# Optimization experiments

Measured on AMD Instinct MI355X. Metric: run time of the kernel, lower is better.

The kernel has to match this reference:

```python
import jax, jax.numpy as jnp
import numpy as np

N_NODES = 100000
N_EDGES = 1600000
IN_CH, HID_CH, OUT_CH = 128, 128, 64


def _glorot(key, shape):
    lim = np.sqrt(6.0 / (shape[0] + shape[1])).astype(np.float32)
    return jax.random.uniform(key, shape, jnp.float32, -lim, lim)


def setup_inputs() -> dict:
    key = jax.random.key(0)
    ks = jax.random.split(key, 11)
    x = jax.random.normal(ks[0], (N_NODES, IN_CH), jnp.float32)
    edge_index = jax.random.randint(ks[1], (2, N_EDGES), 0, N_NODES, dtype=jnp.int64)
    dims = [(IN_CH, HID_CH), (HID_CH, HID_CH), (HID_CH, OUT_CH)]
    params = {}
    for i, (din, dout) in enumerate(dims):
        params[f"Wl{i}"] = _glorot(ks[2 + 3 * i], (din, dout))
        params[f"Wr{i}"] = _glorot(ks[3 + 3 * i], (din, dout))
        params[f"b{i}"] = jnp.zeros((dout,), jnp.float32)
    return {"x": x, "edge_index": edge_index, **params}


def _sage_conv(x, src, dst, Wl, Wr, b):
    # mean aggregation of neighbor (source) features at each destination node
    msg_sum = jax.ops.segment_sum(x[src], dst, num_segments=N_NODES)  # [N, din]
    deg = jax.ops.segment_sum(jnp.ones((src.shape[0],), x.dtype), dst,
                              num_segments=N_NODES)
    mean = msg_sum / jnp.maximum(deg, 1.0)[:, None]
    # lin_l(aggr) + lin_r(self), bias only in lin_l (PyG SAGEConv default)
    return mean @ Wl + x @ Wr + b


def reference(x, edge_index, Wl0, Wr0, b0, Wl1, Wr1, b1, Wl2, Wr2, b2):
    src, dst = edge_index[0], edge_index[1]
    h = jax.nn.relu(_sage_conv(x, src, dst, Wl0, Wr0, b0))  # dropout = identity (eval)
    h = jax.nn.relu(_sage_conv(h, src, dst, Wl1, Wr1, b1))
    out = _sage_conv(h, src, dst, Wl2, Wr2, b2)
    return out
```

## Files before the change

### kernel.cpp

```cpp
#include <hip/hip_runtime.h>
#include <stdint.h>

#define NN 100000
#define NE 1600000
#define NBUK 782
#define G 256
#define CHUNK 6250
#define GCHUNK 512

typedef unsigned int u32;
typedef unsigned short u16;
typedef short v8s __attribute__((ext_vector_type(8)));
typedef float v4f __attribute__((ext_vector_type(4)));

union U4S8 {
    uint4 u;
    v8s s;
};

__device__ __forceinline__ float bf2f(u16 u) {
    return __uint_as_float(((u32)u) << 16);
}
__device__ __forceinline__ u16 f2bf(float f) {
    u32 u = __float_as_uint(f);
    u = u + 0x7FFFu + ((u >> 16) & 1u);
    return (u16)(u >> 16);
}
__device__ __forceinline__ float lo16(u32 u) { return __uint_as_float(u << 16); }
__device__ __forceinline__ float hi16(u32 u) {
    return __uint_as_float(u & 0xFFFF0000u);
}

#define SL ((NN + 1) * 8)

__global__ void detect_kernel(const u32* __restrict__ ei,
                              const u32* __restrict__ x, int* flags) {
    __shared__ int bad64, badbf;
    int t = threadIdx.x;
    if (t == 0) { bad64 = 0; badbf = 0; }
    __syncthreads();
    if (ei[2 * t + 1] != 0u) atomicAdd(&bad64, 1);
    u32 d = x[t];
    u32 e = (d >> 7) & 0xFFu;
    if (e != 0u && (e < 96u || e > 160u)) atomicAdd(&badbf, 1);
    __syncthreads();
    if (t == 0) {
        flags[0] = (bad64 < 16) ? 1 : 0;
        flags[1] = (badbf < 16) ? 1 : 0;
    }
}

__global__ void conv_x(const void* __restrict__ x, const int* __restrict__ flags,
                       u32* __restrict__ xbG, u32* __restrict__ h1G,
                       u32* __restrict__ h2G) {
    int i = blockIdx.x * 256 + threadIdx.x;
    if (i >= (NN + 1) * 64) return;
    int c = i & 7;
    int q = i >> 3;
    int node = q % (NN + 1);
    int g = q / (NN + 1);
    if (node == NN) {
        xbG[i] = 0;
        h1G[i] = 0;
        h2G[i] = 0;
        return;
    }
    int col = g * 8 + c;
    u32 o;
    if (flags[1]) {
        o = ((const u32*)x)[node * 64 + col];
    } else {
        float2 v = ((const float2*)x)[node * 64 + col];
        o = ((u32)f2bf(v.y) << 16) | (u32)f2bf(v.x);
    }
    xbG[i] = o;
}

__global__ void wt_prep_all(const void* __restrict__ Wr0,
                            const void* __restrict__ Wl0,
                            const void* __restrict__ b0,
                            const void* __restrict__ Wr1,
                            const void* __restrict__ Wl1,
                            const void* __restrict__ b1,
                            const void* __restrict__ Wr2,
                            const void* __restrict__ Wl2,
                            const void* __restrict__ b2,
                            const int* __restrict__ flags,
                            u16* __restrict__ WT0, float* __restrict__ bf0,
                            u16* __restrict__ WT1, float* __restrict__ bf1,
                            u16* __restrict__ WT2, float* __restrict__ bf2_) {
    const void* Wr;
    const void* Wl;
    const void* bias;
    u16* WT;
    float* bias_f;
    int cout, t;
    if (blockIdx.x < 128) {
        Wr = Wr0; Wl = Wl0; bias = b0; WT = WT0; bias_f = bf0; cout = 128;
        t = blockIdx.x * 256 + threadIdx.x;
    } else if (blockIdx.x < 256) {
        Wr = Wr1; Wl = Wl1; bias = b1; WT = WT1; bias_f = bf1; cout = 128;
        t = (blockIdx.x - 128) * 256 + threadIdx.x;
    } else {
        Wr = Wr2; Wl = Wl2; bias = b2; WT = WT2; bias_f = bf2_; cout = 64;
        t = (blockIdx.x - 256) * 256 + threadIdx.x;
    }
    if (t < 256 * cout) {
        int k = t / cout, c = t % cout;
        const void* W = (k < 128) ? Wr : Wl;
        int kk = k & 127;
        float v;
        if (flags[1])
            v = bf2f(((const u16*)W)[kk * cout + c]);
        else
            v = ((const float*)W)[kk * cout + c];
        WT[c * 256 + k] = f2bf(v);
    }
    if (t < cout) {
        bias_f[t] =
            flags[1] ? bf2f(((const u16*)bias)[t]) : ((const float*)bias)[t];
    }
}

__global__ __launch_bounds__(256) void p1_hist(const void* __restrict__ ei,
                                               const int* __restrict__ flags,
                                               int* __restrict__ hist) {
    __shared__ int h[NBUK];
    int g = blockIdx.x, t = threadIdx.x;
    for (int b = t; b < NBUK; b += 256) h[b] = 0;
    __syncthreads();
    int e0 = g * CHUNK;
    int e1 = e0 + CHUNK;
    const int* p = (const int*)ei;
    if (flags[0]) {
        for (int e = e0 + t; e < e1; e += 256)
            atomicAdd(&h[p[2 * (NE + e)] >> 7], 1);
    } else {
        for (int e = e0 + t; e < e1; e += 256)
            atomicAdd(&h[p[NE + e] >> 7], 1);
    }
    __syncthreads();
    for (int b = t; b < NBUK; b += 256) hist[b * G + g] = h[b];
}

__global__ void scan_block_g(const int* __restrict__ in, int* __restrict__ out,
                             int* __restrict__ bsums, int n) {
    __shared__ int sS[256];
    int t = threadIdx.x;
    int base = blockIdx.x * 1024 + t * 4;
    int c[4];
#pragma unroll
    for (int i = 0; i < 4; ++i) c[i] = (base + i < n) ? in[base + i] : 0;
    int s = c[0] + c[1] + c[2] + c[3];
    sS[t] = s;
    __syncthreads();
    for (int dlt = 1; dlt < 256; dlt <<= 1) {
        int v = (t >= dlt) ? sS[t - dlt] : 0;
        __syncthreads();
        sS[t] += v;
        __syncthreads();
    }
    int run = sS[t] - s;
    if (t == 255) bsums[blockIdx.x] = sS[255];
#pragma unroll
    for (int i = 0; i < 4; ++i) {
        if (base + i < n) out[base + i] = run;
        run += c[i];
    }
}

__global__ void scan_top_g(int* bsums, int nb) {
    __shared__ int sS[256];
    int t = threadIdx.x;
    int v = (t < nb) ? bsums[t] : 0;
    sS[t] = v;
    __syncthreads();
    for (int d = 1; d < 256; d <<= 1) {
        int u = (t >= d) ? sS[t - d] : 0;
        __syncthreads();
        sS[t] += u;
        __syncthreads();
    }
    if (t < nb) bsums[t] = sS[t] - v;
}

__global__ void scan_add_g(int* __restrict__ out, const int* __restrict__ bsums,
                           int n) {
    int i = blockIdx.x * 256 + threadIdx.x;
    if (i < n) out[i] += bsums[i >> 10];
}

__global__ __launch_bounds__(256) void p2_scatter(const void* __restrict__ ei,
                                                  const int* __restrict__ flags,
                                                  const int* __restrict__ histS,
                                                  int2* __restrict__ ebuf) {
    __shared__ int cur[NBUK];
    int g = blockIdx.x, t = threadIdx.x;
    for (int b = t; b < NBUK; b += 256) cur[b] = histS[b * G + g];
    __syncthreads();
    int e0 = g * CHUNK;
    int e1 = e0 + CHUNK;
    const int* p = (const int*)ei;
    int is64 = flags[0];
    for (int e = e0 + t; e < e1; e += 256) {
        int s, d;
        if (is64) {
            s = p[2 * e];
            d = p[2 * (NE + e)];
        } else {
            s = p[e];
            d = p[NE + e];
        }
        int pos = atomicAdd(&cur[d >> 7], 1);
        ebuf[pos] = make_int2(s, d);
    }
}

__global__ __launch_bounds__(256) void p3_build(const int* __restrict__ histS,
                                                const int2* __restrict__ ebuf,
                                                int* __restrict__ off,
                                                int* __restrict__ ssrc) {
    __shared__ int cnt[128], pref[128], cur[128];
    int b = blockIdx.x, t = threadIdx.x;
    int node0 = b << 7;
    int bs = histS[b * G];
    int be = (b == NBUK - 1) ? NE : histS[(b + 1) * G];
    if (t < 128) cnt[t] = 0;
    __syncthreads();
    for (int e = bs + t; e < be; e += 256)
        atomicAdd(&cnt[ebuf[e].y - node0], 1);
    __syncthreads();
    if (t < 128) pref[t] = cnt[t];
    __syncthreads();
    for (int d = 1; d < 128; d <<= 1) {
        int v = 0;
        if (t < 128 && t >= d) v = pref[t - d];
        __syncthreads();
        if (t < 128) pref[t] += v;
        __syncthreads();
    }
    if (t < 128) {
        int ex = pref[t] - cnt[t];
        cur[t] = ex;
        int node = node0 + t;
        if (node < NN) off[node] = bs + ex;
    }
    if (b == NBUK - 1 && t == 0) off[NN] = NE;
    __syncthreads();
    for (int e = bs + t; e < be; e += 256) {
        int2 sd = ebuf[e];
        int pos = atomicAdd(&cur[sd.y - node0], 1);
        ssrc[bs + pos] = sd.x;
    }
}

__global__ __launch_bounds__(256) void gather_mean_g(
    const u32* __restrict__ featG, const int* __restrict__ off,
    const int* __restrict__ ssrc, u32* __restrict__ meanG) {
    __shared__ int sidx[4][GCHUNK];
    const int g = blockIdx.x & 7;
    const int nb = blockIdx.x >> 3;
    const int wv = threadIdx.x >> 6;
    const int lane = threadIdx.x & 63;
    const int ns = lane >> 2;
    const int c = lane & 3;
    const int node0 = nb * 64 + wv * 16;
    if (node0 >= NN) return;
    const uint2* fg2 = (const uint2*)(featG + (size_t)g * SL);
    u32* mg = meanG + (size_t)g * SL;

    const int e0 = __builtin_amdgcn_readfirstlane(off[node0]);
    const int e1 = __builtin_amdgcn_readfirstlane(off[node0 + 16]);
    const int node = node0 + ns;
    const int myo0 = off[node];
    const int myo1 = off[node + 1];
    const int cnt = myo1 - myo0;

    float a0 = 0.f, a1 = 0.f, a2 = 0.f, a3 = 0.f;
    for (int cb = e0; cb < e1; cb += GCHUNK) {
        const int m = min(GCHUNK, e1 - cb);
#pragma unroll
        for (int r = 0; r < GCHUNK / 64; ++r) {
            int i = r * 64 + lane;
            int v = ssrc[cb + ((i < m) ? i : 0)];
            sidx[wv][i] = v;
        }
        __builtin_amdgcn_s_waitcnt(0);
        __builtin_amdgcn_wave_barrier();
        int s0 = myo0 - cb; s0 = (s0 > 0) ? s0 : 0;
        int s1 = myo1 - cb; s1 = (s1 < m) ? s1 : m;
        int j = s0;
        for (; j + 4 <= s1; j += 4) {
            int i0 = sidx[wv][j];
            int i1 = sidx[wv][j + 1];
            int i2 = sidx[wv][j + 2];
            int i3 = sidx[wv][j + 3];
            uint2 u0 = fg2[(size_t)i0 * 4 + c];
            uint2 u1 = fg2[(size_t)i1 * 4 + c];
            uint2 u2 = fg2[(size_t)i2 * 4 + c];
            uint2 u3 = fg2[(size_t)i3 * 4 + c];
            a0 += lo16(u0.x); a1 += hi16(u0.x);
            a2 += lo16(u0.y); a3 += hi16(u0.y);
            a0 += lo16(u1.x); a1 += hi16(u1.x);
            a2 += lo16(u1.y); a3 += hi16(u1.y);
            a0 += lo16(u2.x); a1 += hi16(u2.x);
            a2 += lo16(u2.y); a3 += hi16(u2.y);
            a0 += lo16(u3.x); a1 += hi16(u3.x);
            a2 += lo16(u3.y); a3 += hi16(u3.y);
        }
        for (; j < s1; ++j) {
            int i0 = sidx[wv][j];
            uint2 u0 = fg2[(size_t)i0 * 4 + c];
            a0 += lo16(u0.x); a1 += hi16(u0.x);
            a2 += lo16(u0.y); a3 += hi16(u0.y);
        }
        __builtin_amdgcn_wave_barrier();
    }
    float inv = 1.0f / (float)(cnt > 0 ? cnt : 1);
    uint2 o;
    o.x = ((u32)f2bf(a1 * inv) << 16) | (u32)f2bf(a0 * inv);
    o.y = ((u32)f2bf(a3 * inv) << 16) | (u32)f2bf(a2 * inv);
    *(uint2*)(mg + (size_t)node * 8 + c * 2) = o;
}

template <int COUT, bool RELU, bool FINAL>
__global__ __launch_bounds__(256, 2) void sage_mfma(
    const u32* __restrict__ selfG, const u32* __restrict__ meanG,
    const u16* __restrict__ WT, const float* __restrict__ bias_f,
    void* __restrict__ out, const int* __restrict__ flags) {
    constexpr int CT = COUT / 16;
    __shared__ u16 wlds[256 * COUT];
    const int tid = threadIdx.x;
    const int wave = tid >> 6;
    const int lane = tid & 63;
    const int n16 = lane & 15;
    const int quad = lane >> 4;
    const int bfin = flags[1];

    {
        const uint4* src = (const uint4*)WT;
        char* wb = (char*)wlds;
        constexpr int NITER = (COUT * 32) / 256;
#pragma unroll
        for (int i = 0; i < NITER; ++i) {
            int idx = i * 256 + tid;
            int c = idx >> 5;
            int off = (idx & 31) << 4;
            *(uint4*)(wb + c * 512 + (off ^ ((c & 7) << 4))) = src[idx];
        }
    }
    __syncthreads();

    const int rowb = blockIdx.x * 256 + wave * 64 + n16;
    const int gq = quad >> 1;
    const int wcol = (quad & 1) * 4;
    int rbase[4];
#pragma unroll
    for (int mt = 0; mt < 4; ++mt) {
        int r = rowb + mt * 16;
        r = (r < NN) ? r : (NN - 1);
        rbase[mt] = r * 8 + gq * SL + wcol;
    }

    v4f acc[4][CT];
#pragma unroll
    for (int mt = 0; mt < 4; ++mt)
#pragma unroll
        for (int ct = 0; ct < CT; ++ct) acc[mt][ct] = (v4f)(0.f);

    const char* wb = (const char*)wlds;
    const int swz = (n16 & 7) << 4;
#pragma unroll
    for (int ks = 0; ks < 8; ++ks) {
        const u32* bp = (ks < 4) ? selfG : meanG;
        const int kof = (ks & 3) * 2 * SL;
        U4S8 nf[4];
#pragma unroll
        for (int mt = 0; mt < 4; ++mt)
            nf[mt].u = *(const uint4*)(bp + kof + rbase[mt]);
        U4S8 wf[CT];
#pragma unroll
        for (int ct = 0; ct < CT; ++ct) {
            int addr = (ct * 16 + n16) * 512 + ((ks * 64 + quad * 16) ^ swz);
            wf[ct].u = *(const uint4*)(wb + addr);
        }
#pragma unroll
        for (int mt = 0; mt < 4; ++mt)
#pragma unroll
            for (int ct = 0; ct < CT; ++ct)
                acc[mt][ct] = __builtin_amdgcn_mfma_f32_16x16x32_bf16(
                    wf[ct].s, nf[mt].s, acc[mt][ct], 0, 0, 0);
    }

    float4 bv[CT];
#pragma unroll
    for (int ct = 0; ct < CT; ++ct)
        bv[ct] = *(const float4*)&bias_f[ct * 16 + quad * 4];

#pragma unroll
    for (int mt = 0; mt < 4; ++mt) {
        int row = rowb + mt * 16;
        if (row < NN) {
#pragma unroll
            for (int ct = 0; ct < CT; ++ct) {
                float v0 = acc[mt][ct][0] + bv[ct].x;
                float v1 = acc[mt][ct][1] + bv[ct].y;
                float v2 = acc[mt][ct][2] + bv[ct].z;
                float v3 = acc[mt][ct][3] + bv[ct].w;
                if (RELU) {
                    v0 = fmaxf(v0, 0.f);
                    v1 = fmaxf(v1, 0.f);
                    v2 = fmaxf(v2, 0.f);
                    v3 = fmaxf(v3, 0.f);
                }
                if (FINAL && !bfin) {
                    float4 o = {v0, v1, v2, v3};
                    *(float4*)((float*)out + (size_t)row * COUT + ct * 16 +
                               quad * 4) = o;
                } else {
                    uint2 o;
                    o.x = (u32)f2bf(v0) | ((u32)f2bf(v1) << 16);
                    o.y = (u32)f2bf(v2) | ((u32)f2bf(v3) << 16);
                    if (FINAL) {
                        *(uint2*)((u16*)out + (size_t)row * COUT + ct * 16 +
                                  quad * 4) = o;
                    } else {
                        *(uint2*)((u32*)out + (size_t)ct * SL + (size_t)row * 8 +
                                  quad * 2) = o;
                    }
                }
            }
        }
    }
}

extern "C" void kernel_launch(void* const* d_in, const int* in_sizes, int n_in,
                              void* d_out, int out_size, void* d_ws,
                              size_t ws_size, hipStream_t stream) {
    const void* x = d_in[0];
    const void* ei = d_in[1];
    const void* Wl0 = d_in[2];
    const void* Wr0 = d_in[3];
    const void* b0 = d_in[4];
    const void* Wl1 = d_in[5];
    const void* Wr1 = d_in[6];
    const void* b1 = d_in[7];
    const void* Wl2 = d_in[8];
    const void* Wr2 = d_in[9];
    const void* b2 = d_in[10];

    char* ws = (char*)d_ws;
    size_t o = 0;
    auto alloc = [&](size_t bytes) {
        void* p = ws + o;
        o = (o + bytes + 511) & ~(size_t)511;
        return p;
    };
    int* flags = (int*)alloc(16);
    int* hist = (int*)alloc((size_t)NBUK * G * 4);
    int* bsums = (int*)alloc(256 * 4);
    int* off = (int*)alloc((NN + 1) * 4);
    int* ssrc = (int*)alloc((size_t)NE * 4);
    int2* ebuf = (int2*)alloc((size_t)NE * 8);
    u32* xb = (u32*)alloc((size_t)(NN + 1) * 64 * 4);
    u32* meanB = (u32*)alloc((size_t)(NN + 1) * 64 * 4);
    u32* h1 = (u32*)alloc((size_t)(NN + 1) * 64 * 4);
    u32* h2 = (u32*)alloc((size_t)(NN + 1) * 64 * 4);
    u16* WT0 = (u16*)alloc(256 * 128 * 2);
    u16* WT1 = (u16*)alloc(256 * 128 * 2);
    u16* WT2 = (u16*)alloc(256 * 64 * 2);
    float* bf0 = (float*)alloc(128 * 4);
    float* bf1 = (float*)alloc(128 * 4);
    float* bf2_ = (float*)alloc(64 * 4);

    constexpr int L = NBUK * G;
    constexpr int NBLK = (L + 1023) / 1024;
    constexpr int RB = (NN + 255) / 256;
    constexpr int GB = 8 * ((NN + 63) / 64);

    detect_kernel<<<1, 256, 0, stream>>>((const u32*)ei, (const u32*)x, flags);
    conv_x<<<((NN + 1) * 64 + 255) / 256, 256, 0, stream>>>(x, flags, xb, h1,
                                                            h2);
    wt_prep_all<<<320, 256, 0, stream>>>(Wr0, Wl0, b0, Wr1, Wl1, b1, Wr2, Wl2,
                                         b2, flags, WT0, bf0, WT1, bf1, WT2,
                                         bf2_);

    p1_hist<<<G, 256, 0, stream>>>(ei, flags, hist);
    scan_block_g<<<NBLK, 256, 0, stream>>>(hist, hist, bsums, L);
    scan_top_g<<<1, 256, 0, stream>>>(bsums, NBLK);
    scan_add_g<<<(L + 255) / 256, 256, 0, stream>>>(hist, bsums, L);
    p2_scatter<<<G, 256, 0, stream>>>(ei, flags, hist, ebuf);
    p3_build<<<NBUK, 256, 0, stream>>>(hist, ebuf, off, ssrc);

    gather_mean_g<<<GB, 256, 0, stream>>>(xb, off, ssrc, meanB);
    sage_mfma<128, true, false><<<RB, 256, 0, stream>>>(xb, meanB, WT0, bf0,
                                                        h1, flags);
    gather_mean_g<<<GB, 256, 0, stream>>>(h1, off, ssrc, meanB);
    sage_mfma<128, true, false><<<RB, 256, 0, stream>>>(h1, meanB, WT1, bf1,
                                                        h2, flags);
    gather_mean_g<<<GB, 256, 0, stream>>>(h2, off, ssrc, meanB);
    sage_mfma<64, false, true><<<RB, 256, 0, stream>>>(h2, meanB, WT2, bf2_,
                                                       d_out, flags);
}
```

Measured before the change: 419.4 us.

## Replace bucketed two-pass CSR build with global atomic count/scatter; unroll gather by 8

Replaces the LDS-bucketed histogram, scatter and per-bucket rebuild with a simple global-atomic per-node degree count, a scan over node counts, and an atomic scatter of sources directly into CSR order. This drops the intermediate int2 edge buffer and one full pass over the edges. The gather kernel now stores byte offsets precomputed with a shift and unrolls the neighbor loop by 8 for more loads in flight. The trade-off is heavy global atomic contention, and neighbor order within each node becomes nondeterministic, which changes float summation order.

```diff
diff --git a/kernel.cpp b/kernel.cpp
--- a/kernel.cpp
+++ b/kernel.cpp
@@ -3,9 +3,6 @@
 
 #define NN 100000
 #define NE 1600000
-#define NBUK 782
-#define G 256
-#define CHUNK 6250
 #define GCHUNK 512
 
 typedef unsigned int u32;
@@ -52,8 +49,9 @@
 
 __global__ void conv_x(const void* __restrict__ x, const int* __restrict__ flags,
                        u32* __restrict__ xbG, u32* __restrict__ h1G,
-                       u32* __restrict__ h2G) {
+                       u32* __restrict__ h2G, int* __restrict__ cnt) {
     int i = blockIdx.x * 256 + threadIdx.x;
+    if (i < NN) cnt[i] = 0;
     if (i >= (NN + 1) * 64) return;
     int c = i & 7;
     int q = i >> 3;
@@ -122,25 +120,16 @@
     }
 }
 
-__global__ __launch_bounds__(256) void p1_hist(const void* __restrict__ ei,
+__global__ __launch_bounds__(256) void e_count(const void* __restrict__ ei,
                                                const int* __restrict__ flags,
-                                               int* __restrict__ hist) {
-    __shared__ int h[NBUK];
-    int g = blockIdx.x, t = threadIdx.x;
-    for (int b = t; b < NBUK; b += 256) h[b] = 0;
-    __syncthreads();
-    int e0 = g * CHUNK;
-    int e1 = e0 + CHUNK;
+                                               int* __restrict__ cnt) {
     const int* p = (const int*)ei;
-    if (flags[0]) {
-        for (int e = e0 + t; e < e1; e += 256)
-            atomicAdd(&h[p[2 * (NE + e)] >> 7], 1);
-    } else {
-        for (int e = e0 + t; e < e1; e += 256)
-            atomicAdd(&h[p[NE + e] >> 7], 1);
-    }
-    __syncthreads();
-    for (int b = t; b < NBUK; b += 256) hist[b * G + g] = h[b];
+    int stride = gridDim.x * 256;
+    int is64 = flags[0];
+    for (int e = blockIdx.x * 256 + threadIdx.x; e < NE; e += stride) {
+        int d = is64 ? p[2 * (NE + e)] : p[NE + e];
+        atomicAdd(&cnt[d], 1);
+    }
 }
 
 __global__ void scan_block_g(const int* __restrict__ in, int* __restrict__ out,
@@ -184,25 +173,25 @@
     if (t < nb) bsums[t] = sS[t] - v;
 }
 
-__global__ void scan_add_g(int* __restrict__ out, const int* __restrict__ bsums,
-                           int n) {
+__global__ void scan_add2(int* __restrict__ off, int* __restrict__ cur,
+                          const int* __restrict__ bsums, int n) {
     int i = blockIdx.x * 256 + threadIdx.x;
-    if (i < n) out[i] += bsums[i >> 10];
-}
-
-__global__ __launch_bounds__(256) void p2_scatter(const void* __restrict__ ei,
-                                                  const int* __restrict__ flags,
-                                                  const int* __restrict__ histS,
-                                                  int2* __restrict__ ebuf) {
-    __shared__ int cur[NBUK];
-    int g = blockIdx.x, t = threadIdx.x;
-    for (int b = t; b < NBUK; b += 256) cur[b] = histS[b * G + g];
-    __syncthreads();
-    int e0 = g * CHUNK;
-    int e1 = e0 + CHUNK;
+    if (i < n) {
+        int v = off[i] + bsums[i >> 10];
+        off[i] = v;
+        cur[i] = v;
+    }
+    if (i == 0) off[n] = NE;
+}
+
+__global__ __launch_bounds__(256) void e_scatter(const void* __restrict__ ei,
+                                                 const int* __restrict__ flags,
+                                                 int* __restrict__ cur,
+                                                 int* __restrict__ ssrc) {
     const int* p = (const int*)ei;
+    int stride = gridDim.x * 256;
     int is64 = flags[0];
-    for (int e = e0 + t; e < e1; e += 256) {
+    for (int e = blockIdx.x * 256 + threadIdx.x; e < NE; e += stride) {
         int s, d;
         if (is64) {
             s = p[2 * e];
@@ -211,53 +200,15 @@
             s = p[e];
             d = p[NE + e];
         }
-        int pos = atomicAdd(&cur[d >> 7], 1);
-        ebuf[pos] = make_int2(s, d);
-    }
-}
-
-__global__ __launch_bounds__(256) void p3_build(const int* __restrict__ histS,
-                                                const int2* __restrict__ ebuf,
-                                                int* __restrict__ off,
-                                                int* __restrict__ ssrc) {
-    __shared__ int cnt[128], pref[128], cur[128];
-    int b = blockIdx.x, t = threadIdx.x;
-    int node0 = b << 7;
-    int bs = histS[b * G];
-    int be = (b == NBUK - 1) ? NE : histS[(b + 1) * G];
-    if (t < 128) cnt[t] = 0;
-    __syncthreads();
-    for (int e = bs + t; e < be; e += 256)
-        atomicAdd(&cnt[ebuf[e].y - node0], 1);
-    __syncthreads();
-    if (t < 128) pref[t] = cnt[t];
-    __syncthreads();
-    for (int d = 1; d < 128; d <<= 1) {
-        int v = 0;
-        if (t < 128 && t >= d) v = pref[t - d];
-        __syncthreads();
-        if (t < 128) pref[t] += v;
-        __syncthreads();
-    }
-    if (t < 128) {
-        int ex = pref[t] - cnt[t];
-        cur[t] = ex;
-        int node = node0 + t;
-        if (node < NN) off[node] = bs + ex;
-    }
-    if (b == NBUK - 1 && t == 0) off[NN] = NE;
-    __syncthreads();
-    for (int e = bs + t; e < be; e += 256) {
-        int2 sd = ebuf[e];
-        int pos = atomicAdd(&cur[sd.y - node0], 1);
-        ssrc[bs + pos] = sd.x;
+        int pos = atomicAdd(&cur[d], 1);
+        ssrc[pos] = s;
     }
 }
 
 __global__ __launch_bounds__(256) void gather_mean_g(
     const u32* __restrict__ featG, const int* __restrict__ off,
     const int* __restrict__ ssrc, u32* __restrict__ meanG) {
-    __shared__ int sidx[4][GCHUNK];
+    __shared__ u32 sidx[4][GCHUNK];
     const int g = blockIdx.x & 7;
     const int nb = blockIdx.x >> 3;
     const int wv = threadIdx.x >> 6;
@@ -266,8 +217,9 @@
     const int c = lane & 3;
     const int node0 = nb * 64 + wv * 16;
     if (node0 >= NN) return;
-    const uint2* fg2 = (const uint2*)(featG + (size_t)g * SL);
+    const char* fgb = (const char*)(featG + (size_t)g * SL);
     u32* mg = meanG + (size_t)g * SL;
+    const u32 coff = (u32)(c * 8);
 
     const int e0 = __builtin_amdgcn_readfirstlane(off[node0]);
     const int e1 = __builtin_amdgcn_readfirstlane(off[node0 + 16]);
@@ -276,13 +228,22 @@
     const int myo1 = off[node + 1];
     const int cnt = myo1 - myo0;
 
+#define LD2(v) (*(const uint2*)(fgb + (size_t)((v) + coff)))
+#define ACC2(u)                    \
+    do {                           \
+        a0 += lo16((u).x);         \
+        a1 += hi16((u).x);         \
+        a2 += lo16((u).y);         \
+        a3 += hi16((u).y);         \
+    } while (0)
+
     float a0 = 0.f, a1 = 0.f, a2 = 0.f, a3 = 0.f;
     for (int cb = e0; cb < e1; cb += GCHUNK) {
         const int m = min(GCHUNK, e1 - cb);
 #pragma unroll
         for (int r = 0; r < GCHUNK / 64; ++r) {
             int i = r * 64 + lane;
-            int v = ssrc[cb + ((i < m) ? i : 0)];
+            u32 v = (u32)ssrc[cb + ((i < m) ? i : 0)] << 5;
             sidx[wv][i] = v;
         }
         __builtin_amdgcn_s_waitcnt(0);
@@ -290,32 +251,46 @@
         int s0 = myo0 - cb; s0 = (s0 > 0) ? s0 : 0;
         int s1 = myo1 - cb; s1 = (s1 < m) ? s1 : m;
         int j = s0;
+        for (; j + 8 <= s1; j += 8) {
+            u32 v0 = sidx[wv][j];
+            u32 v1 = sidx[wv][j + 1];
+            u32 v2 = sidx[wv][j + 2];
+            u32 v3 = sidx[wv][j + 3];
+            u32 v4 = sidx[wv][j + 4];
+            u32 v5 = sidx[wv][j + 5];
+            u32 v6 = sidx[wv][j + 6];
+            u32 v7 = sidx[wv][j + 7];
+            uint2 u0 = LD2(v0);
+            uint2 u1 = LD2(v1);
+            uint2 u2 = LD2(v2);
+            uint2 u3 = LD2(v3);
+            uint2 u4 = LD2(v4);
+            uint2 u5 = LD2(v5);
+            uint2 u6 = LD2(v6);
+            uint2 u7 = LD2(v7);
+            ACC2(u0); ACC2(u1); ACC2(u2); ACC2(u3);
+            ACC2(u4); ACC2(u5); ACC2(u6); ACC2(u7);
+        }
         for (; j + 4 <= s1; j += 4) {
-            int i0 = sidx[wv][j];
-            int i1 = sidx[wv][j + 1];
-            int i2 = sidx[wv][j + 2];
-            int i3 = sidx[wv][j + 3];
-            uint2 u0 = fg2[(size_t)i0 * 4 + c];
-            uint2 u1 = fg2[(size_t)i1 * 4 + c];
-            uint2 u2 = fg2[(size_t)i2 * 4 + c];
-            uint2 u3 = fg2[(size_t)i3 * 4 + c];
-            a0 += lo16(u0.x); a1 += hi16(u0.x);
-            a2 += lo16(u0.y); a3 += hi16(u0.y);
-            a0 += lo16(u1.x); a1 += hi16(u1.x);
-            a2 += lo16(u1.y); a3 += hi16(u1.y);
-            a0 += lo16(u2.x); a1 += hi16(u2.x);
-            a2 += lo16(u2.y); a3 += hi16(u2.y);
-            a0 += lo16(u3.x); a1 += hi16(u3.x);
-            a2 += lo16(u3.y); a3 += hi16(u3.y);
+            u32 v0 = sidx[wv][j];
+            u32 v1 = sidx[wv][j + 1];
+            u32 v2 = sidx[wv][j + 2];
+            u32 v3 = sidx[wv][j + 3];
+            uint2 u0 = LD2(v0);
+            uint2 u1 = LD2(v1);
+            uint2 u2 = LD2(v2);
+            uint2 u3 = LD2(v3);
+            ACC2(u0); ACC2(u1); ACC2(u2); ACC2(u3);
         }
         for (; j < s1; ++j) {
-            int i0 = sidx[wv][j];
-            uint2 u0 = fg2[(size_t)i0 * 4 + c];
-            a0 += lo16(u0.x); a1 += hi16(u0.x);
-            a2 += lo16(u0.y); a3 += hi16(u0.y);
+            u32 v0 = sidx[wv][j];
+            uint2 u0 = LD2(v0);
+            ACC2(u0);
         }
         __builtin_amdgcn_wave_barrier();
     }
+#undef LD2
+#undef ACC2
     float inv = 1.0f / (float)(cnt > 0 ? cnt : 1);
     uint2 o;
     o.x = ((u32)f2bf(a1 * inv) << 16) | (u32)f2bf(a0 * inv);
@@ -457,11 +432,11 @@
         return p;
     };
     int* flags = (int*)alloc(16);
-    int* hist = (int*)alloc((size_t)NBUK * G * 4);
+    int* cnt = (int*)alloc((size_t)NN * 4);
+    int* cur = (int*)alloc((size_t)NN * 4);
     int* bsums = (int*)alloc(256 * 4);
     int* off = (int*)alloc((NN + 1) * 4);
     int* ssrc = (int*)alloc((size_t)NE * 4);
-    int2* ebuf = (int2*)alloc((size_t)NE * 8);
     u32* xb = (u32*)alloc((size_t)(NN + 1) * 64 * 4);
     u32* meanB = (u32*)alloc((size_t)(NN + 1) * 64 * 4);
     u32* h1 = (u32*)alloc((size_t)(NN + 1) * 64 * 4);
@@ -473,24 +448,22 @@
     float* bf1 = (float*)alloc(128 * 4);
     float* bf2_ = (float*)alloc(64 * 4);
 
-    constexpr int L = NBUK * G;
-    constexpr int NBLK = (L + 1023) / 1024;
+    constexpr int NBLK2 = (NN + 1023) / 1024;
     constexpr int RB = (NN + 255) / 256;
     constexpr int GB = 8 * ((NN + 63) / 64);
 
     detect_kernel<<<1, 256, 0, stream>>>((const u32*)ei, (const u32*)x, flags);
     conv_x<<<((NN + 1) * 64 + 255) / 256, 256, 0, stream>>>(x, flags, xb, h1,
-                                                            h2);
+                                                            h2, cnt);
     wt_prep_all<<<320, 256, 0, stream>>>(Wr0, Wl0, b0, Wr1, Wl1, b1, Wr2, Wl2,
                                          b2, flags, WT0, bf0, WT1, bf1, WT2,
                                          bf2_);
 
-    p1_hist<<<G, 256, 0, stream>>>(ei, flags, hist);
-    scan_block_g<<<NBLK, 256, 0, stream>>>(hist, hist, bsums, L);
-    scan_top_g<<<1, 256, 0, stream>>>(bsums, NBLK);
-    scan_add_g<<<(L + 255) / 256, 256, 0, stream>>>(hist, bsums, L);
-    p2_scatter<<<G, 256, 0, stream>>>(ei, flags, hist, ebuf);
-    p3_build<<<NBUK, 256, 0, stream>>>(hist, ebuf, off, ssrc);
+    e_count<<<2048, 256, 0, stream>>>(ei, flags, cnt);
+    scan_block_g<<<NBLK2, 256, 0, stream>>>(cnt, off, bsums, NN);
+    scan_top_g<<<1, 256, 0, stream>>>(bsums, NBLK2);
+    scan_add2<<<(NN + 255) / 256, 256, 0, stream>>>(off, cur, bsums, NN);
+    e_scatter<<<2048, 256, 0, stream>>>(ei, flags, cur, ssrc);
 
     gather_mean_g<<<GB, 256, 0, stream>>>(xb, off, ssrc, meanB);
     sage_mfma<128, true, false><<<RB, 256, 0, stream>>>(xb, meanB, WT0, bf0,
```

Measured after the change: 577.7 us. +37.8%, slower.
